# Optimization experiments

Hardware: AMD Instinct MI355X
Metric: run time of the kernel (lower is better)

## Reference

```python
import jax, jax.numpy as jnp
import numpy as np

N = 100          # num_objects
H = 128          # decoder_hidden
D = 128          # input_size (== H, required by the module's GRU linears)
REL = 7          # num_relative_features (use_3d=False)
E = N * (N - 1)  # fully-connected, no self loops
B = 32

_mask = ~np.eye(N, dtype=bool)
_SEND_NP, _RECV_NP = np.where(_mask)  # torch.where(~eye): rows=send, cols=recv
SEND = jnp.asarray(_SEND_NP, dtype=jnp.int32)
RECV = jnp.asarray(_RECV_NP, dtype=jnp.int32)


def setup_inputs() -> dict:
    key = jax.random.key(0)
    ks = jax.random.split(key, 34)
    def w(k, shape, scale=0.05):
        return jax.random.normal(k, shape, dtype=jnp.float32) * scale
    inp = {
        "inputs": jax.random.normal(ks[0], (B, N, D), jnp.float32),
        "edge_attr": jax.random.normal(ks[1], (B, E, REL + D), jnp.float32),
        "hidden": jax.random.normal(ks[2], (B, N, H), jnp.float32),
        # msg_mlp: Linear(2H,H) Tanh Linear(H,H) Tanh
        "msg_w1": w(ks[3], (2 * H, H)), "msg_b1": w(ks[4], (H,)),
        "msg_w2": w(ks[5], (H, H)),     "msg_b2": w(ks[6], (H,)),
        # present_msg_mlp: Linear(REL+D,H) ReLU Linear(H,H) ReLU
        "pm_w1": w(ks[7], (REL + D, H)), "pm_b1": w(ks[8], (H,)),
        "pm_w2": w(ks[9], (H, H)),       "pm_b2": w(ks[10], (H,)),
        # res_mlp: Linear(D,H) ReLU Linear(H,H) ReLU
        "res_w1": w(ks[11], (D, H)), "res_b1": w(ks[12], (H,)),
        "res_w2": w(ks[13], (H, H)), "res_b2": w(ks[14], (H,)),
        # GRU-style gates
        "ir_w": w(ks[15], (H, H)), "ir_b": w(ks[16], (H,)),
        "ii_w": w(ks[17], (H, H)), "ii_b": w(ks[18], (H,)),
        "in_w": w(ks[19], (H, H)), "in_b": w(ks[20], (H,)),
        "hr_w": w(ks[21], (H, H)),
        "hi_w": w(ks[22], (H, H)),
        "hh_w": w(ks[23], (H, H)),
        # out_mlp: Linear(H,H) ReLU Linear(H,H) ReLU Linear(H,D)
        "out_w1": w(ks[24], (H, H)), "out_b1": w(ks[25], (H,)),
        "out_w2": w(ks[26], (H, H)), "out_b2": w(ks[27], (H,)),
        "out_w3": w(ks[28], (H, D)), "out_b3": w(ks[29], (D,)),
    }
    return inp


def _scatter_mean(msgs, recv, num_nodes):
    # msgs: [B, E, H] -> [B, N, H], mean over incoming edges per node
    counts = jnp.zeros((num_nodes,), msgs.dtype).at[recv].add(1.0)
    summed = jnp.zeros((msgs.shape[0], num_nodes, msgs.shape[-1]), msgs.dtype)
    summed = summed.at[:, recv].add(msgs)
    return summed / counts[None, :, None]


def reference(inputs, edge_attr, hidden,
              msg_w1, msg_b1, msg_w2, msg_b2,
              pm_w1, pm_b1, pm_w2, pm_b2,
              res_w1, res_b1, res_w2, res_b2,
              ir_w, ir_b, ii_w, ii_b, in_w, in_b,
              hr_w, hi_w, hh_w,
              out_w1, out_b1, out_w2, out_b2, out_w3, out_b3):
    # gather hidden states along edges (dropout is identity: p=0 / eval)
    hm = jnp.concatenate([hidden[:, RECV], hidden[:, SEND]], axis=-1)  # [B,E,2H]
    hm = jnp.tanh(jnp.tanh(hm @ msg_w1 + msg_b1) @ msg_w2 + msg_b2)
    hidden_node = _scatter_mean(hm, RECV, N)                           # [B,N,H]

    pm = jax.nn.relu(jax.nn.relu(edge_attr @ pm_w1 + pm_b1) @ pm_w2 + pm_b2)
    present_node = _scatter_mean(pm, RECV, N)
    present_node = present_node + jax.nn.relu(
        jax.nn.relu(inputs @ res_w1 + res_b1) @ res_w2 + res_b2)

    r = jax.nn.sigmoid(present_node @ ir_w + ir_b + hidden_node @ hr_w)
    i = jax.nn.sigmoid(present_node @ ii_w + ii_b + hidden_node @ hi_w)
    n = jnp.tanh(present_node @ in_w + in_b + r * (hidden_node @ hh_w))
    hidden_new = (1.0 - i) * n + i * hidden

    pred = jax.nn.relu(hidden_new @ out_w1 + out_b1)
    pred = jax.nn.relu(pred @ out_w2 + out_b2)
    pred = pred @ out_w3 + out_b3
    return pred, hidden_new
```

## Files before the change

### kernel.cpp

```cpp
#include <hip/hip_runtime.h>

typedef unsigned short u16;
typedef unsigned int   u32;
typedef __attribute__((ext_vector_type(8))) short bf8;
typedef __attribute__((ext_vector_type(4))) float f4;

#define DF __device__ __forceinline__

DF float bf2f(u16 h){ u32 u = ((u32)h) << 16; float f; __builtin_memcpy(&f, &u, 4); return f; }
DF u16 f2bf(float f){ u32 u; __builtin_memcpy(&u, &f, 4); u = (u + 0x7FFFu + ((u >> 16) & 1u)) >> 16; return (u16)u; }
DF float fexp2(float x){ return __builtin_amdgcn_exp2f(x); }
DF float frcp (float x){ return __builtin_amdgcn_rcpf(x); }
DF float tanhF(float x){ float e = fexp2(2.8853900817779268f * x); return 1.0f - 2.0f * frcp(e + 1.0f); }
DF float sigF (float x){ return frcp(1.0f + fexp2(-1.4426950408889634f * x)); }
DF float4 ld4u(const float* p){ float4 v; __builtin_memcpy(&v, p, 16); return v; }
DF u32 cvtpk(float lo, float hi){ u32 r; asm("v_cvt_pk_bf16_f32 %0, %1, %2" : "=v"(r) : "v"(lo), "v"(hi)); return r; }

DF const bf8* fragp(const u16* packed, int w, int nt, int ks, int lane){
  return reinterpret_cast<const bf8*>(packed + (((w * 32 + nt * 4 + ks) * 64 + lane) * 8));
}
DF const bf8* fragp_pm1(const u16* packed, int nt, int ks, int lane){
  return reinterpret_cast<const bf8*>(packed + (((512 + nt * 5 + ks) * 64 + lane) * 8));
}

struct WPtrs { const float* p[16]; };

__global__ __launch_bounds__(256) void k_pack(WPtrs wp, u16* __restrict__ packed){
  int bi = blockIdx.x;
  int lane = threadIdx.x & 63, warp = threadIdx.x >> 6;
  if(bi == 16){
    const float* __restrict__ src = wp.p[14];
    u16* __restrict__ dst = packed + 512 * 64 * 8;
    for(int i = warp; i < 40; i += 4){
      int nt = i / 5, ks = i - nt * 5;
      int col = nt * 16 + (lane & 15);
      int kb  = ks * 32 + (lane >> 4) * 8;
      u16* o = dst + (i * 64 + lane) * 8;
      for(int j = 0; j < 8; j++){
        int row = kb + j;
        o[j] = (row < 135) ? f2bf(src[row * 128 + col]) : (u16)0;
      }
    }
    return;
  }
  const float* __restrict__ src = wp.p[bi];
  u16* __restrict__ dst = packed + bi * 32 * 64 * 8;
  for(int i = warp; i < 32; i += 4){
    int nt = i >> 2, ks = i & 3;
    int col = nt * 16 + (lane & 15);
    int kb  = ks * 32 + (lane >> 4) * 8;
    u16* o = dst + (i * 64 + lane) * 8;
    for(int j = 0; j < 8; j++) o[j] = f2bf(src[(kb + j) * 128 + col]);
  }
}

__global__ __launch_bounds__(512) void k_node_pre(
    const float* __restrict__ hidden, const float* __restrict__ inputs,
    const u16* __restrict__ packed,
    const float* __restrict__ res_b1, const float* __restrict__ res_b2,
    float* __restrict__ Ptop, float* __restrict__ Pbot, float* __restrict__ res2)
{
  __shared__ __align__(16) u16 hid[64 * 136];
  __shared__ __align__(16) u16 inp[64 * 136];
  __shared__ __align__(16) u16 t1s[64 * 136];
  int row0 = blockIdx.x * 64;
  int t = threadIdx.x, lane = t & 63, w = t >> 6;
  int lrow = lane & 15, lk = lane >> 4;
  for(int i = t; i < 64 * 128; i += 512){
    int rr = i >> 7, cc = i & 127;
    hid[rr * 136 + cc] = f2bf(hidden[(row0 + rr) * 128 + cc]);
    inp[rr * 136 + cc] = f2bf(inputs[(row0 + rr) * 128 + cc]);
  }
  bf8 f0[4], f1[4], f5[4], f6[4];
  #pragma unroll
  for(int k = 0; k < 4; k++){
    f0[k] = *fragp(packed, 0, w, k, lane);
    f1[k] = *fragp(packed, 1, w, k, lane);
    f5[k] = *fragp(packed, 5, w, k, lane);
    f6[k] = *fragp(packed, 6, w, k, lane);
  }
  int col = w * 16 + lrow;
  float rb1 = res_b1[col], rb2 = res_b2[col];
  __syncthreads();
  #pragma unroll
  for(int m = 0; m < 4; m++){
    bf8 a[4], a2[4];
    #pragma unroll
    for(int k = 0; k < 4; k++){
      a[k]  = *reinterpret_cast<const bf8*>(&hid[(m * 16 + lrow) * 136 + k * 32 + lk * 8]);
      a2[k] = *reinterpret_cast<const bf8*>(&inp[(m * 16 + lrow) * 136 + k * 32 + lk * 8]);
    }
    f4 c0 = {0.f,0.f,0.f,0.f}, c1 = {0.f,0.f,0.f,0.f}, c2 = {0.f,0.f,0.f,0.f};
    #pragma unroll
    for(int k = 0; k < 4; k++){
      c0 = __builtin_amdgcn_mfma_f32_16x16x32_bf16(a[k],  f0[k], c0, 0, 0, 0);
      c1 = __builtin_amdgcn_mfma_f32_16x16x32_bf16(a[k],  f1[k], c1, 0, 0, 0);
      c2 = __builtin_amdgcn_mfma_f32_16x16x32_bf16(a2[k], f5[k], c2, 0, 0, 0);
    }
    #pragma unroll
    for(int q = 0; q < 4; q++){
      int gr = row0 + m * 16 + lk * 4 + q;
      Ptop[gr * 128 + col] = c0[q];
      Pbot[gr * 128 + col] = c1[q];
      float v = c2[q] + rb1; v = v > 0.f ? v : 0.f;
      t1s[(m * 16 + lk * 4 + q) * 136 + col] = f2bf(v);
    }
  }
  __syncthreads();
  #pragma unroll
  for(int m = 0; m < 4; m++){
    bf8 a3[4];
    #pragma unroll
    for(int k = 0; k < 4; k++)
      a3[k] = *reinterpret_cast<const bf8*>(&t1s[(m * 16 + lrow) * 136 + k * 32 + lk * 8]);
    f4 c = {0.f,0.f,0.f,0.f};
    #pragma unroll
    for(int k = 0; k < 4; k++)
      c = __builtin_amdgcn_mfma_f32_16x16x32_bf16(a3[k], f6[k], c, 0, 0, 0);
    #pragma unroll
    for(int q = 0; q < 4; q++){
      float v = c[q] + rb2; v = v > 0.f ? v : 0.f;
      res2[(row0 + m * 16 + lk * 4 + q) * 128 + col] = v;
    }
  }
}

__global__ __launch_bounds__(256, 4) void k_edge(
    const float* __restrict__ EA,
    const float* __restrict__ Ptop, const float* __restrict__ Pbot,
    const float* __restrict__ msg_b1, const float* __restrict__ msg_b2,
    const float* __restrict__ pm_b1, const float* __restrict__ pm_b2,
    const u16* __restrict__ packed,
    float* __restrict__ hnode, float* __restrict__ pnode)
{
  __shared__ __align__(16) u16 buf[112 * 160];
  char* bufb = (char*)buf;
  int bid = blockIdx.x;
  bool isPM = (bid & 1) == 0;
  int blk = bid >> 1;
  int b = blk / 100, r = blk - b * 100;
  int t = threadIdx.x, lane = t & 63, w = t >> 6;
  int lrow = lane & 15, lk = lane >> 4;
  int n0 = 2 * w, n1 = 2 * w + 1;

  if(isPM){
    bf8 w1a[5], w1b[5], w2a[4], w2b[4];
    #pragma unroll
    for(int k = 0; k < 5; k++){ w1a[k] = *fragp_pm1(packed, n0, k, lane); w1b[k] = *fragp_pm1(packed, n1, k, lane); }
    #pragma unroll
    for(int k = 0; k < 4; k++){ w2a[k] = *fragp(packed, 15, n0, k, lane); w2b[k] = *fragp(packed, 15, n1, k, lane); }
    float b1a = pm_b1[n0 * 16 + lrow], b1b = pm_b1[n1 * 16 + lrow];
    float b2a = pm_b2[n0 * 16 + lrow], b2b = pm_b2[n1 * 16 + lrow];
    for(int i = t; i < 99 * 20; i += 256){
      int row = i / 20, g = i - row * 20;
      int s = row + (row >= r ? 1 : 0);
      int e = s * 99 + (r < s ? r : r - 1);
      const float* rp = EA + ((size_t)b * 9900 + e) * 135 + g * 8;
      u32 p0 = 0, p1 = 0, p2 = 0, p3 = 0;
      int off;
      if(g < 16){
        float4 v0 = ld4u(rp), v1 = ld4u(rp + 4);
        p0 = cvtpk(v0.x, v0.y); p1 = cvtpk(v0.z, v0.w);
        p2 = cvtpk(v1.x, v1.y); p3 = cvtpk(v1.z, v1.w);
        off = row * 320 + ((g * 16) ^ ((row & 7) << 4));
      } else {
        if(g == 16){
          float4 v0 = ld4u(rp);
          p0 = cvtpk(v0.x, v0.y); p1 = cvtpk(v0.z, v0.w);
          p2 = cvtpk(rp[4], rp[5]); p3 = cvtpk(rp[6], 0.f);
        }
        off = row * 320 + g * 16;
      }
      u32 pk[4] = {p0, p1, p2, p3};
      *reinterpret_cast<uint4*>(bufb + off) = *reinterpret_cast<const uint4*>(pk);
    }
    __syncthreads();
    #pragma unroll
    for(int m = 0; m < 7; m++){
      int arow = m * 16 + lrow;
      bf8 a[5];
      #pragma unroll
      for(int k = 0; k < 4; k++)
        a[k] = *reinterpret_cast<const bf8*>(bufb + arow * 320 + ((k * 64 + lk * 16) ^ ((arow & 7) << 4)));
      a[4] = *reinterpret_cast<const bf8*>(bufb + arow * 320 + 256 + lk * 16);
      f4 c0 = {0.f,0.f,0.f,0.f}, c1 = {0.f,0.f,0.f,0.f};
      #pragma unroll
      for(int k = 0; k < 5; k++){
        c0 = __builtin_amdgcn_mfma_f32_16x16x32_bf16(a[k], w1a[k], c0, 0, 0, 0);
        c1 = __builtin_amdgcn_mfma_f32_16x16x32_bf16(a[k], w1b[k], c1, 0, 0, 0);
      }
      __syncthreads();
      #pragma unroll
      for(int q = 0; q < 4; q++){
        int row = m * 16 + lk * 4 + q;
        float v0 = c0[q] + b1a; v0 = v0 > 0.f ? v0 : 0.f;
        float v1 = c1[q] + b1b; v1 = v1 > 0.f ? v1 : 0.f;
        int sw = (row & 7) << 4;
        *reinterpret_cast<u16*>(bufb + row * 320 + (((n0 * 16 + lrow) * 2) ^ sw)) = f2bf(v0);
        *reinterpret_cast<u16*>(bufb + row * 320 + (((n1 * 16 + lrow) * 2) ^ sw)) = f2bf(v1);
      }
    }
    __syncthreads();
    float acc0 = 0.f, acc1 = 0.f;
    #pragma unroll
    for(int m = 0; m < 7; m++){
      int arow = m * 16 + lrow;
      bf8 a[4];
      #pragma unroll
      for(int k = 0; k < 4; k++)
        a[k] = *reinterpret_cast<const bf8*>(bufb + arow * 320 + ((k * 64 + lk * 16) ^ ((arow & 7) << 4)));
      f4 c0 = {0.f,0.f,0.f,0.f}, c1 = {0.f,0.f,0.f,0.f};
      #pragma unroll
      for(int k = 0; k < 4; k++){
        c0 = __builtin_amdgcn_mfma_f32_16x16x32_bf16(a[k], w2a[k], c0, 0, 0, 0);
        c1 = __builtin_amdgcn_mfma_f32_16x16x32_bf16(a[k], w2b[k], c1, 0, 0, 0);
      }
      #pragma unroll
      for(int q = 0; q < 4; q++){
        int rr = m * 16 + lk * 4 + q;
        if(rr < 99){
          float v0 = c0[q] + b2a; acc0 += (v0 > 0.f ? v0 : 0.f);
          float v1 = c1[q] + b2b; acc1 += (v1 > 0.f ? v1 : 0.f);
        }
      }
    }
    acc0 += __shfl_xor(acc0, 16); acc0 += __shfl_xor(acc0, 32);
    acc1 += __shfl_xor(acc1, 16); acc1 += __shfl_xor(acc1, 32);
    if(lane < 16){
      float* dst = pnode + ((size_t)b * 100 + r) * 128;
      dst[n0 * 16 + lane] = acc0 * (1.0f / 99.0f);
      dst[n1 * 16 + lane] = acc1 * (1.0f / 99.0f);
    }
  } else {
    bf8 w2a[4], w2b[4];
    #pragma unroll
    for(int k = 0; k < 4; k++){ w2a[k] = *fragp(packed, 13, n0, k, lane); w2b[k] = *fragp(packed, 13, n1, k, lane); }
    float b2a = msg_b2[n0 * 16 + lrow], b2b = msg_b2[n1 * 16 + lrow];
    int c4 = t & 31;
    float4 pt = *reinterpret_cast<const float4*>(Ptop + ((size_t)b * 100 + r) * 128 + c4 * 4);
    float4 mb = *reinterpret_cast<const float4*>(msg_b1 + c4 * 4);
    pt.x += mb.x; pt.y += mb.y; pt.z += mb.z; pt.w += mb.w;
    for(int row = t >> 5; row < 99; row += 8){
      int s = row + (row >= r ? 1 : 0);
      float4 v = *reinterpret_cast<const float4*>(Pbot + ((size_t)b * 100 + s) * 128 + c4 * 4);
      u32 p0 = cvtpk(tanhF(pt.x + v.x), tanhF(pt.y + v.y));
      u32 p1 = cvtpk(tanhF(pt.z + v.z), tanhF(pt.w + v.w));
      int off = row * 320 + ((c4 * 8) ^ ((row & 7) << 4));
      u32 pk[2] = {p0, p1};
      *reinterpret_cast<uint2*>(bufb + off) = *reinterpret_cast<const uint2*>(pk);
    }
    __syncthreads();
    float acc0 = 0.f, acc1 = 0.f;
    #pragma unroll
    for(int m = 0; m < 7; m++){
      int arow = m * 16 + lrow;
      bf8 a[4];
      #pragma unroll
      for(int k = 0; k < 4; k++)
        a[k] = *reinterpret_cast<const bf8*>(bufb + arow * 320 + ((k * 64 + lk * 16) ^ ((arow & 7) << 4)));
      f4 c0 = {0.f,0.f,0.f,0.f}, c1 = {0.f,0.f,0.f,0.f};
      #pragma unroll
      for(int k = 0; k < 4; k++){
        c0 = __builtin_amdgcn_mfma_f32_16x16x32_bf16(a[k], w2a[k], c0, 0, 0, 0);
        c1 = __builtin_amdgcn_mfma_f32_16x16x32_bf16(a[k], w2b[k], c1, 0, 0, 0);
      }
      #pragma unroll
      for(int q = 0; q < 4; q++){
        int rr = m * 16 + lk * 4 + q;
        if(rr < 99){
          acc0 += tanhF(c0[q] + b2a);
          acc1 += tanhF(c1[q] + b2b);
        }
      }
    }
    acc0 += __shfl_xor(acc0, 16); acc0 += __shfl_xor(acc0, 32);
    acc1 += __shfl_xor(acc1, 16); acc1 += __shfl_xor(acc1, 32);
    if(lane < 16){
      float* dst = hnode + ((size_t)b * 100 + r) * 128;
      dst[n0 * 16 + lane] = acc0 * (1.0f / 99.0f);
      dst[n1 * 16 + lane] = acc1 * (1.0f / 99.0f);
    }
  }
}

__global__ __launch_bounds__(512) void k_final(
    const float* __restrict__ hnode, const float* __restrict__ pnode,
    const float* __restrict__ res2, const float* __restrict__ hidden,
    const u16* __restrict__ packed,
    const float* __restrict__ ir_b, const float* __restrict__ ii_b, const float* __restrict__ in_b,
    const float* __restrict__ ob1, const float* __restrict__ ob2, const float* __restrict__ ob3,
    float* __restrict__ out_pred, float* __restrict__ out_hid)
{
  __shared__ __align__(16) u16 hn[64 * 136];
  __shared__ __align__(16) u16 pr[64 * 136];
  __shared__ __align__(16) u16 hw[64 * 136];
  int row0 = blockIdx.x * 64;
  int t = threadIdx.x, lane = t & 63, w = t >> 6;
  int lrow = lane & 15, lk = lane >> 4;
  for(int i = t; i < 64 * 128; i += 512){
    int rr = i >> 7, cc = i & 127;
    hn[rr * 136 + cc] = f2bf(hnode[(row0 + rr) * 128 + cc]);
    pr[rr * 136 + cc] = f2bf(pnode[(row0 + rr) * 128 + cc] + res2[(row0 + rr) * 128 + cc]);
  }
  int col = w * 16 + lrow;
  bf8 mhr[4], mhi[4], mhh[4], mir[4], mii[4], min_[4];
  #pragma unroll
  for(int k = 0; k < 4; k++){
    mhr[k]  = *fragp(packed, 2, w, k, lane);
    mhi[k]  = *fragp(packed, 3, w, k, lane);
    mhh[k]  = *fragp(packed, 4, w, k, lane);
    mir[k]  = *fragp(packed, 7, w, k, lane);
    mii[k]  = *fragp(packed, 8, w, k, lane);
    min_[k] = *fragp(packed, 9, w, k, lane);
  }
  float bir = ir_b[col], bii = ii_b[col], bin = in_b[col];
  __syncthreads();
  #pragma unroll
  for(int m = 0; m < 4; m++){
    bf8 a[4], p[4];
    #pragma unroll
    for(int k = 0; k < 4; k++){
      a[k] = *reinterpret_cast<const bf8*>(&hn[(m * 16 + lrow) * 136 + k * 32 + lk * 8]);
      p[k] = *reinterpret_cast<const bf8*>(&pr[(m * 16 + lrow) * 136 + k * 32 + lk * 8]);
    }
    f4 cR = {0.f,0.f,0.f,0.f}, cI = {0.f,0.f,0.f,0.f}, cN = {0.f,0.f,0.f,0.f};
    f4 dR = {0.f,0.f,0.f,0.f}, dI = {0.f,0.f,0.f,0.f}, dN = {0.f,0.f,0.f,0.f};
    #pragma unroll
    for(int k = 0; k < 4; k++){
      cR = __builtin_amdgcn_mfma_f32_16x16x32_bf16(a[k], mhr[k],  cR, 0, 0, 0);
      cI = __builtin_amdgcn_mfma_f32_16x16x32_bf16(a[k], mhi[k],  cI, 0, 0, 0);
      cN = __builtin_amdgcn_mfma_f32_16x16x32_bf16(a[k], mhh[k],  cN, 0, 0, 0);
      dR = __builtin_amdgcn_mfma_f32_16x16x32_bf16(p[k], mir[k],  dR, 0, 0, 0);
      dI = __builtin_amdgcn_mfma_f32_16x16x32_bf16(p[k], mii[k],  dI, 0, 0, 0);
      dN = __builtin_amdgcn_mfma_f32_16x16x32_bf16(p[k], min_[k], dN, 0, 0, 0);
    }
    #pragma unroll
    for(int q = 0; q < 4; q++){
      int gr = row0 + m * 16 + lk * 4 + q;
      float rv = sigF(dR[q] + bir + cR[q]);
      float iv = sigF(dI[q] + bii + cI[q]);
      float nv = tanhF(dN[q] + bin + rv * cN[q]);
      float hold = hidden[gr * 128 + col];
      float hnew = (1.f - iv) * nv + iv * hold;
      out_hid[gr * 128 + col] = hnew;
      hw[(m * 16 + lk * 4 + q) * 136 + col] = f2bf(hnew);
    }
  }
  __syncthreads();
  {
    bf8 m10[4];
    #pragma unroll
    for(int k = 0; k < 4; k++) m10[k] = *fragp(packed, 10, w, k, lane);
    float bb = ob1[col];
    #pragma unroll
    for(int m = 0; m < 4; m++){
      f4 c = {0.f,0.f,0.f,0.f};
      #pragma unroll
      for(int k = 0; k < 4; k++){
        bf8 a = *reinterpret_cast<const bf8*>(&hw[(m * 16 + lrow) * 136 + k * 32 + lk * 8]);
        c = __builtin_amdgcn_mfma_f32_16x16x32_bf16(a, m10[k], c, 0, 0, 0);
      }
      #pragma unroll
      for(int q = 0; q < 4; q++){
        float v = c[q] + bb; v = v > 0.f ? v : 0.f;
        hn[(m * 16 + lk * 4 + q) * 136 + col] = f2bf(v);
      }
    }
  }
  __syncthreads();
  {
    bf8 m11[4];
    #pragma unroll
    for(int k = 0; k < 4; k++) m11[k] = *fragp(packed, 11, w, k, lane);
    float bb = ob2[col];
    #pragma unroll
    for(int m = 0; m < 4; m++){
      f4 c = {0.f,0.f,0.f,0.f};
      #pragma unroll
      for(int k = 0; k < 4; k++){
        bf8 a = *reinterpret_cast<const bf8*>(&hn[(m * 16 + lrow) * 136 + k * 32 + lk * 8]);
        c = __builtin_amdgcn_mfma_f32_16x16x32_bf16(a, m11[k], c, 0, 0, 0);
      }
      #pragma unroll
      for(int q = 0; q < 4; q++){
        float v = c[q] + bb; v = v > 0.f ? v : 0.f;
        pr[(m * 16 + lk * 4 + q) * 136 + col] = f2bf(v);
      }
    }
  }
  __syncthreads();
  {
    bf8 m12[4];
    #pragma unroll
    for(int k = 0; k < 4; k++) m12[k] = *fragp(packed, 12, w, k, lane);
    float bb = ob3[col];
    #pragma unroll
    for(int m = 0; m < 4; m++){
      f4 c = {0.f,0.f,0.f,0.f};
      #pragma unroll
      for(int k = 0; k < 4; k++){
        bf8 a = *reinterpret_cast<const bf8*>(&pr[(m * 16 + lrow) * 136 + k * 32 + lk * 8]);
        c = __builtin_amdgcn_mfma_f32_16x16x32_bf16(a, m12[k], c, 0, 0, 0);
      }
      #pragma unroll
      for(int q = 0; q < 4; q++)
        out_pred[(row0 + m * 16 + lk * 4 + q) * 128 + col] = c[q] + bb;
    }
  }
}

extern "C" void kernel_launch(void* const* d_in, const int* in_sizes, int n_in,
                              void* d_out, int out_size, void* d_ws, size_t ws_size,
                              hipStream_t stream)
{
  const float* inputs = (const float*)d_in[0];
  const float* edge   = (const float*)d_in[1];
  const float* hidden = (const float*)d_in[2];
  const float* msg_w1 = (const float*)d_in[3];
  const float* msg_b1 = (const float*)d_in[4];
  const float* msg_w2 = (const float*)d_in[5];
  const float* msg_b2 = (const float*)d_in[6];
  const float* pm_w1  = (const float*)d_in[7];
  const float* pm_b1  = (const float*)d_in[8];
  const float* pm_w2  = (const float*)d_in[9];
  const float* pm_b2  = (const float*)d_in[10];
  const float* res_w1 = (const float*)d_in[11];
  const float* res_b1 = (const float*)d_in[12];
  const float* res_w2 = (const float*)d_in[13];
  const float* res_b2 = (const float*)d_in[14];
  const float* ir_w = (const float*)d_in[15]; const float* ir_b = (const float*)d_in[16];
  const float* ii_w = (const float*)d_in[17]; const float* ii_b = (const float*)d_in[18];
  const float* in_w = (const float*)d_in[19]; const float* in_b = (const float*)d_in[20];
  const float* hr_w = (const float*)d_in[21];
  const float* hi_w = (const float*)d_in[22];
  const float* hh_w = (const float*)d_in[23];
  const float* out_w1 = (const float*)d_in[24]; const float* out_b1 = (const float*)d_in[25];
  const float* out_w2 = (const float*)d_in[26]; const float* out_b2 = (const float*)d_in[27];
  const float* out_w3 = (const float*)d_in[28]; const float* out_b3 = (const float*)d_in[29];

  char* ws = (char*)d_ws;
  u16*   packed = (u16*)ws;
  float* Ptop   = (float*)(ws + (1 << 20));
  float* Pbot   = (float*)(ws + (1 << 20) + 1 * 1638400);
  float* res2   = (float*)(ws + (1 << 20) + 2 * 1638400);
  float* hnode  = (float*)(ws + (1 << 20) + 3 * 1638400);
  float* pnode  = (float*)(ws + (1 << 20) + 4 * 1638400);

  WPtrs wp;
  wp.p[0]  = msg_w1;
  wp.p[1]  = msg_w1 + 128 * 128;
  wp.p[2]  = hr_w;  wp.p[3]  = hi_w;  wp.p[4]  = hh_w;
  wp.p[5]  = res_w1; wp.p[6] = res_w2;
  wp.p[7]  = ir_w;  wp.p[8]  = ii_w;  wp.p[9]  = in_w;
  wp.p[10] = out_w1; wp.p[11] = out_w2; wp.p[12] = out_w3;
  wp.p[13] = msg_w2; wp.p[14] = pm_w1; wp.p[15] = pm_w2;

  k_pack<<<17, 256, 0, stream>>>(wp, packed);
  k_node_pre<<<50, 512, 0, stream>>>(hidden, inputs, packed, res_b1, res_b2, Ptop, Pbot, res2);
  k_edge<<<6400, 256, 0, stream>>>(edge, Ptop, Pbot, msg_b1, msg_b2, pm_b1, pm_b2,
                                   packed, hnode, pnode);
  float* outp = (float*)d_out;
  k_final<<<50, 512, 0, stream>>>(hnode, pnode, res2, hidden, packed,
                                  ir_b, ii_b, in_b, out_b1, out_b2, out_b3,
                                  outp, outp + 32 * 100 * 128);
}
```

Before: 136.4 us.

## Merge PM and message edge paths into one block per node with compact LDS

Each block now runs both the present-message MLP and the hidden-message MLP for one (batch, receiver) node in sequence, instead of separate blocks for each path. This halves the grid to 3200 blocks. The LDS tile shrinks from 320-byte rows to 256-byte rows, with a separate small tail buffer for the 7 leftover feature columns, and launch bounds are raised to 5 blocks per CU. The aim is to raise occupancy and cut per-block overhead, but each block now does twice the serial work and adds an extra barrier between the two phases.

```diff
diff --git a/kernel.cpp b/kernel.cpp
--- a/kernel.cpp
+++ b/kernel.cpp
@@ -125,7 +125,7 @@
   }
 }
 
-__global__ __launch_bounds__(256, 4) void k_edge(
+__global__ __launch_bounds__(256, 5) void k_edge(
     const float* __restrict__ EA,
     const float* __restrict__ Ptop, const float* __restrict__ Pbot,
     const float* __restrict__ msg_b1, const float* __restrict__ msg_b2,
@@ -133,82 +133,87 @@
     const u16* __restrict__ packed,
     float* __restrict__ hnode, float* __restrict__ pnode)
 {
-  __shared__ __align__(16) u16 buf[112 * 160];
-  char* bufb = (char*)buf;
-  int bid = blockIdx.x;
-  bool isPM = (bid & 1) == 0;
-  int blk = bid >> 1;
+  __shared__ __align__(16) u16 bufA[112 * 128];
+  __shared__ __align__(16) u16 tail[112 * 8];
+  char* bb = (char*)bufA;
+  char* tb = (char*)tail;
+  int blk = blockIdx.x;
   int b = blk / 100, r = blk - b * 100;
   int t = threadIdx.x, lane = t & 63, w = t >> 6;
   int lrow = lane & 15, lk = lane >> 4;
   int n0 = 2 * w, n1 = 2 * w + 1;
 
-  if(isPM){
-    bf8 w1a[5], w1b[5], w2a[4], w2b[4];
+  {
+    bf8 w1a[5], w1b[5];
     #pragma unroll
     for(int k = 0; k < 5; k++){ w1a[k] = *fragp_pm1(packed, n0, k, lane); w1b[k] = *fragp_pm1(packed, n1, k, lane); }
-    #pragma unroll
-    for(int k = 0; k < 4; k++){ w2a[k] = *fragp(packed, 15, n0, k, lane); w2b[k] = *fragp(packed, 15, n1, k, lane); }
     float b1a = pm_b1[n0 * 16 + lrow], b1b = pm_b1[n1 * 16 + lrow];
-    float b2a = pm_b2[n0 * 16 + lrow], b2b = pm_b2[n1 * 16 + lrow];
-    for(int i = t; i < 99 * 20; i += 256){
-      int row = i / 20, g = i - row * 20;
+    for(int i = t; i < 99 * 16; i += 256){
+      int row = i >> 4, g = i & 15;
       int s = row + (row >= r ? 1 : 0);
       int e = s * 99 + (r < s ? r : r - 1);
-      const float* rp = EA + ((size_t)b * 9900 + e) * 135 + g * 8;
-      u32 p0 = 0, p1 = 0, p2 = 0, p3 = 0;
-      int off;
-      if(g < 16){
-        float4 v0 = ld4u(rp), v1 = ld4u(rp + 4);
-        p0 = cvtpk(v0.x, v0.y); p1 = cvtpk(v0.z, v0.w);
-        p2 = cvtpk(v1.x, v1.y); p3 = cvtpk(v1.z, v1.w);
-        off = row * 320 + ((g * 16) ^ ((row & 7) << 4));
-      } else {
-        if(g == 16){
-          float4 v0 = ld4u(rp);
-          p0 = cvtpk(v0.x, v0.y); p1 = cvtpk(v0.z, v0.w);
-          p2 = cvtpk(rp[4], rp[5]); p3 = cvtpk(rp[6], 0.f);
-        }
-        off = row * 320 + g * 16;
-      }
-      u32 pk[4] = {p0, p1, p2, p3};
-      *reinterpret_cast<uint4*>(bufb + off) = *reinterpret_cast<const uint4*>(pk);
+      const float* rp = EA + ((size_t)(b * 9900 + e)) * 135 + g * 8;
+      float4 v0 = ld4u(rp), v1 = ld4u(rp + 4);
+      u32 pk[4] = {cvtpk(v0.x, v0.y), cvtpk(v0.z, v0.w), cvtpk(v1.x, v1.y), cvtpk(v1.z, v1.w)};
+      *reinterpret_cast<uint4*>(bb + row * 256 + ((g ^ (row & 7)) << 4)) = *reinterpret_cast<const uint4*>(pk);
+    }
+    for(int row = t; row < 99; row += 256){
+      int s = row + (row >= r ? 1 : 0);
+      int e = s * 99 + (r < s ? r : r - 1);
+      const float* rp = EA + ((size_t)(b * 9900 + e)) * 135 + 128;
+      float4 v0 = ld4u(rp);
+      u32 pk[4] = {cvtpk(v0.x, v0.y), cvtpk(v0.z, v0.w), cvtpk(rp[4], rp[5]), cvtpk(rp[6], 0.f)};
+      *reinterpret_cast<uint4*>(tb + row * 16) = *reinterpret_cast<const uint4*>(pk);
     }
     __syncthreads();
     #pragma unroll
     for(int m = 0; m < 7; m++){
       int arow = m * 16 + lrow;
+      int sw = (arow & 7);
       bf8 a[5];
       #pragma unroll
       for(int k = 0; k < 4; k++)
-        a[k] = *reinterpret_cast<const bf8*>(bufb + arow * 320 + ((k * 64 + lk * 16) ^ ((arow & 7) << 4)));
-      a[4] = *reinterpret_cast<const bf8*>(bufb + arow * 320 + 256 + lk * 16);
+        a[k] = *reinterpret_cast<const bf8*>(bb + arow * 256 + (((k * 4 + lk) ^ sw) << 4));
+      bf8 a4 = {0,0,0,0,0,0,0,0};
+      if(lk == 0) a4 = *reinterpret_cast<const bf8*>(tb + arow * 16);
       f4 c0 = {0.f,0.f,0.f,0.f}, c1 = {0.f,0.f,0.f,0.f};
       #pragma unroll
-      for(int k = 0; k < 5; k++){
+      for(int k = 0; k < 4; k++){
         c0 = __builtin_amdgcn_mfma_f32_16x16x32_bf16(a[k], w1a[k], c0, 0, 0, 0);
         c1 = __builtin_amdgcn_mfma_f32_16x16x32_bf16(a[k], w1b[k], c1, 0, 0, 0);
       }
+      c0 = __builtin_amdgcn_mfma_f32_16x16x32_bf16(a4, w1a[4], c0, 0, 0, 0);
+      c1 = __builtin_amdgcn_mfma_f32_16x16x32_bf16(a4, w1b[4], c1, 0, 0, 0);
       __syncthreads();
       #pragma unroll
-      for(int q = 0; q < 4; q++){
-        int row = m * 16 + lk * 4 + q;
-        float v0 = c0[q] + b1a; v0 = v0 > 0.f ? v0 : 0.f;
-        float v1 = c1[q] + b1b; v1 = v1 > 0.f ? v1 : 0.f;
-        int sw = (row & 7) << 4;
-        *reinterpret_cast<u16*>(bufb + row * 320 + (((n0 * 16 + lrow) * 2) ^ sw)) = f2bf(v0);
-        *reinterpret_cast<u16*>(bufb + row * 320 + (((n1 * 16 + lrow) * 2) ^ sw)) = f2bf(v1);
+      for(int qp = 0; qp < 2; qp++){
+        float v0 = c0[2*qp]   + b1a; v0 = v0 > 0.f ? v0 : 0.f;
+        float u0 = c0[2*qp+1] + b1a; u0 = u0 > 0.f ? u0 : 0.f;
+        float v1 = c1[2*qp]   + b1b; v1 = v1 > 0.f ? v1 : 0.f;
+        float u1 = c1[2*qp+1] + b1b; u1 = u1 > 0.f ? u1 : 0.f;
+        u32 p0 = cvtpk(v0, u0), p1 = cvtpk(v1, u1);
+        int row0_ = m * 16 + lk * 4 + 2 * qp;
+        int sw0 = (row0_ & 7) << 4, sw1 = ((row0_ + 1) & 7) << 4;
+        *reinterpret_cast<u16*>(bb + row0_ * 256       + (((n0 * 16 + lrow) * 2) ^ sw0)) = (u16)p0;
+        *reinterpret_cast<u16*>(bb + (row0_ + 1) * 256 + (((n0 * 16 + lrow) * 2) ^ sw1)) = (u16)(p0 >> 16);
+        *reinterpret_cast<u16*>(bb + row0_ * 256       + (((n1 * 16 + lrow) * 2) ^ sw0)) = (u16)p1;
+        *reinterpret_cast<u16*>(bb + (row0_ + 1) * 256 + (((n1 * 16 + lrow) * 2) ^ sw1)) = (u16)(p1 >> 16);
       }
     }
     __syncthreads();
+    bf8 w2a[4], w2b[4];
+    #pragma unroll
+    for(int k = 0; k < 4; k++){ w2a[k] = *fragp(packed, 15, n0, k, lane); w2b[k] = *fragp(packed, 15, n1, k, lane); }
+    float b2a = pm_b2[n0 * 16 + lrow], b2b = pm_b2[n1 * 16 + lrow];
     float acc0 = 0.f, acc1 = 0.f;
     #pragma unroll
     for(int m = 0; m < 7; m++){
       int arow = m * 16 + lrow;
+      int sw = (arow & 7);
       bf8 a[4];
       #pragma unroll
       for(int k = 0; k < 4; k++)
-        a[k] = *reinterpret_cast<const bf8*>(bufb + arow * 320 + ((k * 64 + lk * 16) ^ ((arow & 7) << 4)));
+        a[k] = *reinterpret_cast<const bf8*>(bb + arow * 256 + (((k * 4 + lk) ^ sw) << 4));
       f4 c0 = {0.f,0.f,0.f,0.f}, c1 = {0.f,0.f,0.f,0.f};
       #pragma unroll
       for(int k = 0; k < 4; k++){
@@ -231,7 +236,10 @@
       dst[n0 * 16 + lane] = acc0 * (1.0f / 99.0f);
       dst[n1 * 16 + lane] = acc1 * (1.0f / 99.0f);
     }
-  } else {
+  }
+  __syncthreads();
+
+  {
     bf8 w2a[4], w2b[4];
     #pragma unroll
     for(int k = 0; k < 4; k++){ w2a[k] = *fragp(packed, 13, n0, k, lane); w2b[k] = *fragp(packed, 13, n1, k, lane); }
@@ -243,21 +251,20 @@
     for(int row = t >> 5; row < 99; row += 8){
       int s = row + (row >= r ? 1 : 0);
       float4 v = *reinterpret_cast<const float4*>(Pbot + ((size_t)b * 100 + s) * 128 + c4 * 4);
-      u32 p0 = cvtpk(tanhF(pt.x + v.x), tanhF(pt.y + v.y));
-      u32 p1 = cvtpk(tanhF(pt.z + v.z), tanhF(pt.w + v.w));
-      int off = row * 320 + ((c4 * 8) ^ ((row & 7) << 4));
-      u32 pk[2] = {p0, p1};
-      *reinterpret_cast<uint2*>(bufb + off) = *reinterpret_cast<const uint2*>(pk);
+      u32 pk[2] = {cvtpk(tanhF(pt.x + v.x), tanhF(pt.y + v.y)),
+                   cvtpk(tanhF(pt.z + v.z), tanhF(pt.w + v.w))};
+      *reinterpret_cast<uint2*>(bb + row * 256 + ((8 * c4) ^ ((row & 7) << 4))) = *reinterpret_cast<const uint2*>(pk);
     }
     __syncthreads();
     float acc0 = 0.f, acc1 = 0.f;
     #pragma unroll
     for(int m = 0; m < 7; m++){
       int arow = m * 16 + lrow;
+      int sw = (arow & 7);
       bf8 a[4];
       #pragma unroll
       for(int k = 0; k < 4; k++)
-        a[k] = *reinterpret_cast<const bf8*>(bufb + arow * 320 + ((k * 64 + lk * 16) ^ ((arow & 7) << 4)));
+        a[k] = *reinterpret_cast<const bf8*>(bb + arow * 256 + (((k * 4 + lk) ^ sw) << 4));
       f4 c0 = {0.f,0.f,0.f,0.f}, c1 = {0.f,0.f,0.f,0.f};
       #pragma unroll
       for(int k = 0; k < 4; k++){
@@ -457,7 +464,7 @@
 
   k_pack<<<17, 256, 0, stream>>>(wp, packed);
   k_node_pre<<<50, 512, 0, stream>>>(hidden, inputs, packed, res_b1, res_b2, Ptop, Pbot, res2);
-  k_edge<<<6400, 256, 0, stream>>>(edge, Ptop, Pbot, msg_b1, msg_b2, pm_b1, pm_b2,
+  k_edge<<<3200, 256, 0, stream>>>(edge, Ptop, Pbot, msg_b1, msg_b2, pm_b1, pm_b2,
                                    packed, hnode, pnode);
   float* outp = (float*)d_out;
   k_final<<<50, 512, 0, stream>>>(hnode, pnode, res2, hidden, packed,
```

Result: slower. 141.3 us (+3.6%).
